# Optimization experiments

Hardware: AMD Instinct MI355X
Metric: run time of the kernel (lower is better)

## Reference

```python
import jax, jax.numpy as jnp
import numpy as np

KH = KW = 5  # receptive field


def _pair_w(a, b):
    # a, b: [...] in [0,1] -> soft one-hot over the 2-bit address (a = high bit): [..., 4]
    sa = jnp.stack([1.0 - a, a], axis=-1)
    sb = jnp.stack([1.0 - b, b], axis=-1)
    return (sa[..., :, None] * sb[..., None, :]).reshape(*a.shape, 4)


def _lut_nodes(g, lut):
    # g: [N, T, M, 6] node inputs in [0,1]; lut: [T, M, 64] raw LUT params.
    # DWN-style differentiable LUT: out = sum_a sigmoid(lut[a]) * prod_j (x_j if bit_j else 1-x_j)
    T, M = lut.shape[0], lut.shape[1]
    p = jax.nn.sigmoid(lut).reshape(T, M, 4, 4, 4)  # bits grouped pairwise, MSB-first
    Wa = _pair_w(g[..., 0], g[..., 1])  # [N,T,M,4]
    Wb = _pair_w(g[..., 2], g[..., 3])
    Wc = _pair_w(g[..., 4], g[..., 5])
    return jnp.einsum('tmpqr,ntmp,ntmq,ntmr->ntm', p, Wa, Wb, Wc)


def _lut_layer(h, idx, lut):
    # h: [N, T, P] previous-layer activations per tree; idx: [T, M, 6] in [0,P)
    T = idx.shape[0]
    g = h[:, jnp.arange(T)[:, None, None], idx]  # gather: [N, T, M, 6]
    return _lut_nodes(g, lut)


def setup_inputs() -> dict:
    key = jax.random.key(0)
    ks = jax.random.split(key, 7)
    x = jax.random.uniform(ks[0], (64, 1, 8, 8), dtype=jnp.float32)
    idx0 = jax.random.randint(ks[1], (128, 36, 6), 0, 25, dtype=jnp.int32)
    lut0 = jax.random.normal(ks[2], (128, 36, 64), dtype=jnp.float32)
    idx1 = jax.random.randint(ks[3], (128, 6, 6), 0, 36, dtype=jnp.int32)
    lut1 = jax.random.normal(ks[4], (128, 6, 64), dtype=jnp.float32)
    idx2 = jax.random.randint(ks[5], (128, 1, 6), 0, 6, dtype=jnp.int32)
    lut2 = jax.random.normal(ks[6], (128, 1, 64), dtype=jnp.float32)
    return dict(x=x, idx0=idx0, lut0=lut0, idx1=idx1, lut1=lut1, idx2=idx2, lut2=lut2)


def reference(x, idx0, lut0, idx1, lut1, idx2, lut2):
    B, C, H, W = x.shape
    oh, ow = H - KH + 1, W - KW + 1  # stride 1, padding 0 (as in nn.Unfold here)
    # im2col unfold, channel-major then (kh, kw) -- matches nn.Unfold ordering
    patches = jnp.stack(
        [x[:, c, i:i + oh, j:j + ow] for c in range(C) for i in range(KH) for j in range(KW)],
        axis=1,
    )  # [B, C*KH*KW, oh, ow]
    feat = patches.reshape(B, C * KH * KW, oh * ow).transpose(0, 2, 1).reshape(-1, C * KH * KW)  # [N, 25]
    # layer 0: gather from shared patch features into every tree
    g0 = feat[:, idx0]                      # [N, T, 36, 6]
    h0 = _lut_nodes(g0, lut0)               # [N, T, 36]
    h1 = _lut_layer(h0, idx1, lut1)         # [N, T, 6]
    h2 = _lut_layer(h1, idx2, lut2)         # [N, T, 1]
    T = lut0.shape[0]
    out = h2[..., 0].reshape(B, oh * ow, T).transpose(0, 2, 1).reshape(B, T, oh, ow)
    return out
```

## Files before the change

### kernel.cpp

```cpp
#include <hip/hip_runtime.h>
#include <hip/hip_fp16.h>

#define T_TREES 128
#define M0 36
#define M1 6
#define NNODES 43
#define XPAD 67
#define SLUT_ELEMS (T_TREES * NNODES * 64)

typedef float v2f __attribute__((ext_vector_type(2)));

__device__ __forceinline__ float sigmoidf(float v) {
    return 1.f / (1.f + __expf(-v));
}

__global__ __launch_bounds__(256) void sig_kernel(
    const float* __restrict__ lut0, const float* __restrict__ lut1,
    const float* __restrict__ lut2, float* __restrict__ slut) {
    int i4 = blockIdx.x * 256 + threadIdx.x;
    int j4 = i4 & 15;
    int tn = i4 >> 4;
    int t = tn / NNODES;
    int node = tn - t * NNODES;
    const float4* src;
    if (node < M0)            src = (const float4*)lut0 + (t * M0 + node) * 16 + j4;
    else if (node < M0 + M1)  src = (const float4*)lut1 + (t * M1 + (node - M0)) * 16 + j4;
    else                      src = (const float4*)lut2 + t * 16 + j4;
    float4 v = *src;
    float4 r;
    r.x = sigmoidf(v.x); r.y = sigmoidf(v.y);
    r.z = sigmoidf(v.z); r.w = sigmoidf(v.w);
    reinterpret_cast<float4*>(slut)[i4] = r;
}

__device__ __forceinline__ void pair_w(v2f a, v2f b, v2f w[4]) {
    v2f ab = a * b;
    w[3] = ab;
    w[2] = a - ab;
    w[1] = b - ab;
    w[0] = (1.f - a) - w[1];
}

__device__ __forceinline__ v2f lut_node_v2(const float* __restrict__ P,
                                           v2f a, v2f b, v2f c,
                                           v2f d, v2f e, v2f f) {
    v2f wa[4], wb[4], wc[4];
    pair_w(a, b, wa);
    pair_w(c, d, wb);
    pair_w(e, f, wc);
    v2f acc = {0.f, 0.f};
#pragma unroll
    for (int p = 0; p < 4; ++p) {
        v2f tp = {0.f, 0.f};
#pragma unroll
        for (int q = 0; q < 4; ++q) {
            const float* Pq = P + p * 16 + q * 4;
            v2f tq = Pq[0] * wc[0] + Pq[1] * wc[1] + Pq[2] * wc[2] + Pq[3] * wc[3];
            tp += tq * wb[q];
        }
        acc += tp * wa[p];
    }
    return acc;
}

__device__ __forceinline__ void hoist_P(const float* __restrict__ src, float P[64]) {
#pragma unroll
    for (int i = 0; i < 16; ++i) {
        float4 v = reinterpret_cast<const float4*>(src)[i];
        P[4 * i] = v.x; P[4 * i + 1] = v.y; P[4 * i + 2] = v.z; P[4 * i + 3] = v.w;
    }
}

__global__ __launch_bounds__(256, 4) void fused_kernel(
    const float* __restrict__ x,
    const int* __restrict__ idx0, const int* __restrict__ idx1,
    const int* __restrict__ idx2, const float* __restrict__ slut,
    float* __restrict__ out) {
    __shared__ float xs[8 * XPAD];
    __shared__ __half2 h0s[M0 * 64];
    __shared__ __align__(8) float h1s[M1 * 128];

    const int tid = threadIdx.x;
    const int bx = blockIdx.x;
    const int t = bx & 127;
    const int e = bx >> 7;

    const float* __restrict__ xq = x + e * 512;
    for (int i = tid; i < 512; i += 256)
        xs[(i >> 6) * XPAD + (i & 63)] = xq[i];
    __syncthreads();

    const int w = __builtin_amdgcn_readfirstlane(tid >> 6);
    const int ln = tid & 63;
    const float* __restrict__ slt = slut + t * (NNODES * 64);

#pragma unroll 1
    for (int k = 0; k < 9; ++k) {
        const int m = w * 9 + k;
        float P[64];
        hoist_P(slt + m * 64, P);
        const int* id = idx0 + (t * M0 + m) * 6;
        int di[6];
#pragma unroll
        for (int j = 0; j < 6; ++j) {
            int kk = id[j];
            int ii = (kk * 13) >> 6;
            di[j] = kk - 5 * ii + ii * 8;
        }
        int b = ln >> 3;
        int s = (ln & 7) * 2;
        int xb = b * XPAD + (s >> 2) * 8 + (s & 3);
        v2f g[6];
#pragma unroll
        for (int j = 0; j < 6; ++j) {
            int a0 = xb + di[j];
            g[j].x = xs[a0];
            g[j].y = xs[a0 + 1];
        }
        v2f r = lut_node_v2(P, g[0], g[1], g[2], g[3], g[4], g[5]);
        h0s[m * 64 + ln] = __floats2half2_rn(r.x, r.y);
    }
    __syncthreads();

#pragma unroll 1
    for (int m1 = w; m1 < M1; m1 += 4) {
        float P[64];
        hoist_P(slt + (M0 + m1) * 64, P);
        const int* id = idx1 + (t * M1 + m1) * 6;
        v2f g[6];
#pragma unroll
        for (int j = 0; j < 6; ++j) {
            float2 f = __half22float2(h0s[id[j] * 64 + ln]);
            g[j].x = f.x; g[j].y = f.y;
        }
        v2f r = lut_node_v2(P, g[0], g[1], g[2], g[3], g[4], g[5]);
        *reinterpret_cast<v2f*>(h1s + m1 * 128 + 2 * ln) = r;
    }
    __syncthreads();

    if (tid < 64) {
        float P[64];
        hoist_P(slt + (M0 + M1) * 64, P);
        const int* id = idx2 + t * 6;
        int rl = 2 * tid;
        v2f g[6];
#pragma unroll
        for (int j = 0; j < 6; ++j)
            g[j] = *reinterpret_cast<const v2f*>(h1s + id[j] * 128 + rl);
        v2f o = lut_node_v2(P, g[0], g[1], g[2], g[3], g[4], g[5]);
        int row = e * 128 + rl;
        int b = row >> 4, s = row & 15;
        *reinterpret_cast<v2f*>(out + b * (T_TREES * 16) + t * 16 + s) = o;
    }
}

__global__ __launch_bounds__(256, 2) void fused_fb_kernel(
    const float* __restrict__ x,
    const int* __restrict__ idx0, const float* __restrict__ lut0,
    const int* __restrict__ idx1, const float* __restrict__ lut1,
    const int* __restrict__ idx2, const float* __restrict__ lut2,
    float* __restrict__ out) {
    __shared__ float xs[16 * XPAD];
    __shared__ __align__(16) float Ps[NNODES * 64];
    __shared__ __half2 h0s[M0 * 128];
    __shared__ __align__(8) float h1s[M1 * 256];

    const int tid = threadIdx.x;
    const int bx = blockIdx.x;
    const int t = bx & 127;
    const int q = bx >> 7;

    const float* __restrict__ xq = x + q * 1024;
    for (int i = tid; i < 1024; i += 256)
        xs[(i >> 6) * XPAD + (i & 63)] = xq[i];
    for (int i = tid; i < NNODES * 64; i += 256) {
        float v;
        if (i < M0 * 64)              v = lut0[t * (M0 * 64) + i];
        else if (i < (M0 + M1) * 64)  v = lut1[t * (M1 * 64) + (i - M0 * 64)];
        else                          v = lut2[t * 64 + (i - (M0 + M1) * 64)];
        Ps[i] = sigmoidf(v);
    }
    __syncthreads();

    const int w = tid >> 6, ln = tid & 63;
#pragma unroll 1
    for (int k = 0; k < 9; ++k) {
        const int m = w * 9 + k;
        float P[64];
        hoist_P(Ps + m * 64, P);
        const int* id = idx0 + (t * M0 + m) * 6;
        int di[6];
#pragma unroll
        for (int j = 0; j < 6; ++j) {
            int kk = id[j];
            int ii = (kk * 13) >> 6;
            di[j] = kk - 5 * ii + ii * 8;
        }
#pragma unroll
        for (int u = 0; u < 2; ++u) {
            int p = u * 64 + ln;
            int b = p >> 3;
            int s = (p & 7) * 2;
            int xb = b * XPAD + (s >> 2) * 8 + (s & 3);
            v2f g[6];
#pragma unroll
            for (int j = 0; j < 6; ++j) {
                int a0 = xb + di[j];
                g[j].x = xs[a0];
                g[j].y = xs[a0 + 1];
            }
            v2f r = lut_node_v2(P, g[0], g[1], g[2], g[3], g[4], g[5]);
            h0s[m * 128 + p] = __floats2half2_rn(r.x, r.y);
        }
    }
    __syncthreads();
#pragma unroll 1
    for (int m1 = w; m1 < M1; m1 += 4) {
        float P[64];
        hoist_P(Ps + (M0 + m1) * 64, P);
        const int* id = idx1 + (t * M1 + m1) * 6;
#pragma unroll
        for (int u = 0; u < 2; ++u) {
            int p = u * 64 + ln;
            v2f g[6];
#pragma unroll
            for (int j = 0; j < 6; ++j) {
                float2 f = __half22float2(h0s[id[j] * 128 + p]);
                g[j].x = f.x; g[j].y = f.y;
            }
            v2f r = lut_node_v2(P, g[0], g[1], g[2], g[3], g[4], g[5]);
            *reinterpret_cast<v2f*>(h1s + m1 * 256 + 2 * p) = r;
        }
    }
    __syncthreads();
    if (tid < 128) {
        float P[64];
        hoist_P(Ps + (M0 + M1) * 64, P);
        const int* id = idx2 + t * 6;
        int rl = 2 * tid;
        v2f g[6];
#pragma unroll
        for (int j = 0; j < 6; ++j)
            g[j] = *reinterpret_cast<const v2f*>(h1s + id[j] * 256 + rl);
        v2f o = lut_node_v2(P, g[0], g[1], g[2], g[3], g[4], g[5]);
        int row = q * 256 + rl;
        int b = row >> 4, s = row & 15;
        *reinterpret_cast<v2f*>(out + b * (T_TREES * 16) + t * 16 + s) = o;
    }
}

extern "C" void kernel_launch(void* const* d_in, const int* in_sizes, int n_in,
                              void* d_out, int out_size, void* d_ws, size_t ws_size,
                              hipStream_t stream) {
    const float* x    = (const float*)d_in[0];
    const int*   idx0 = (const int*)  d_in[1];
    const float* lut0 = (const float*)d_in[2];
    const int*   idx1 = (const int*)  d_in[3];
    const float* lut1 = (const float*)d_in[4];
    const int*   idx2 = (const int*)  d_in[5];
    const float* lut2 = (const float*)d_in[6];
    float* out = (float*)d_out;

    if (ws_size >= (size_t)SLUT_ELEMS * sizeof(float)) {
        float* slut = (float*)d_ws;
        sig_kernel<<<SLUT_ELEMS / 4 / 256, 256, 0, stream>>>(lut0, lut1, lut2, slut);
        fused_kernel<<<dim3(8 * T_TREES), 256, 0, stream>>>(
            x, idx0, idx1, idx2, slut, out);
    } else {
        fused_fb_kernel<<<dim3(4 * T_TREES), 256, 0, stream>>>(
            x, idx0, lut0, idx1, lut1, idx2, lut2, out);
    }
}
```

Before: 24.25 us.

## Fuse sigmoid LUT precompute into main kernel with per-block workspace slice

Removes the separate sigmoid kernel launch. Each block now computes sigmoid of its tree's LUT parameters into its own slice of workspace memory, then reads them back through global memory. Blocks are halved and each handles twice the pixels, with two pixel groups per lane. This cuts one kernel launch and its dependency, but every block redundantly recomputes sigmoids (4x per tree). It also relies on a block fence so the block's own global writes are visible to its threads.

After: 23.79 us. About the same (-1.9%).

```diff
diff --git a/kernel.cpp b/kernel.cpp
--- a/kernel.cpp
+++ b/kernel.cpp
@@ -5,32 +5,13 @@
 #define M0 36
 #define M1 6
 #define NNODES 43
+#define TREE_SL (NNODES * 64)
 #define XPAD 67
-#define SLUT_ELEMS (T_TREES * NNODES * 64)
 
 typedef float v2f __attribute__((ext_vector_type(2)));
 
 __device__ __forceinline__ float sigmoidf(float v) {
     return 1.f / (1.f + __expf(-v));
-}
-
-__global__ __launch_bounds__(256) void sig_kernel(
-    const float* __restrict__ lut0, const float* __restrict__ lut1,
-    const float* __restrict__ lut2, float* __restrict__ slut) {
-    int i4 = blockIdx.x * 256 + threadIdx.x;
-    int j4 = i4 & 15;
-    int tn = i4 >> 4;
-    int t = tn / NNODES;
-    int node = tn - t * NNODES;
-    const float4* src;
-    if (node < M0)            src = (const float4*)lut0 + (t * M0 + node) * 16 + j4;
-    else if (node < M0 + M1)  src = (const float4*)lut1 + (t * M1 + (node - M0)) * 16 + j4;
-    else                      src = (const float4*)lut2 + t * 16 + j4;
-    float4 v = *src;
-    float4 r;
-    r.x = sigmoidf(v.x); r.y = sigmoidf(v.y);
-    r.z = sigmoidf(v.z); r.w = sigmoidf(v.w);
-    reinterpret_cast<float4*>(slut)[i4] = r;
 }
 
 __device__ __forceinline__ void pair_w(v2f a, v2f b, v2f w[4]) {
@@ -71,34 +52,44 @@
     }
 }
 
-__global__ __launch_bounds__(256, 4) void fused_kernel(
+__global__ __launch_bounds__(256) void fused_kernel(
     const float* __restrict__ x,
-    const int* __restrict__ idx0, const int* __restrict__ idx1,
-    const int* __restrict__ idx2, const float* __restrict__ slut,
-    float* __restrict__ out) {
-    __shared__ float xs[8 * XPAD];
-    __shared__ __half2 h0s[M0 * 64];
-    __shared__ __align__(8) float h1s[M1 * 128];
+    const int* __restrict__ idx0, const float* __restrict__ lut0,
+    const int* __restrict__ idx1, const float* __restrict__ lut1,
+    const int* __restrict__ idx2, const float* __restrict__ lut2,
+    float* __restrict__ ws_slut, float* __restrict__ out) {
+    __shared__ float xs[16 * XPAD];
+    __shared__ __half2 h0s[M0 * 128];
+    __shared__ __align__(8) float h1s[M1 * 256];
 
     const int tid = threadIdx.x;
     const int bx = blockIdx.x;
     const int t = bx & 127;
-    const int e = bx >> 7;
-
-    const float* __restrict__ xq = x + e * 512;
-    for (int i = tid; i < 512; i += 256)
+    const int q = bx >> 7;
+
+    float* __restrict__ slb = ws_slut + (size_t)bx * TREE_SL;
+
+    const float* __restrict__ xq = x + q * 1024;
+    for (int i = tid; i < 1024; i += 256)
         xs[(i >> 6) * XPAD + (i & 63)] = xq[i];
+    for (int i = tid; i < TREE_SL; i += 256) {
+        float v;
+        if (i < M0 * 64)              v = lut0[t * (M0 * 64) + i];
+        else if (i < (M0 + M1) * 64)  v = lut1[t * (M1 * 64) + (i - M0 * 64)];
+        else                          v = lut2[t * 64 + (i - (M0 + M1) * 64)];
+        slb[i] = sigmoidf(v);
+    }
+    __threadfence_block();
     __syncthreads();
 
     const int w = __builtin_amdgcn_readfirstlane(tid >> 6);
     const int ln = tid & 63;
-    const float* __restrict__ slt = slut + t * (NNODES * 64);
 
 #pragma unroll 1
     for (int k = 0; k < 9; ++k) {
         const int m = w * 9 + k;
         float P[64];
-        hoist_P(slt + m * 64, P);
+        hoist_P(slb + m * 64, P);
         const int* id = idx0 + (t * M0 + m) * 6;
         int di[6];
 #pragma unroll
@@ -107,48 +98,56 @@
             int ii = (kk * 13) >> 6;
             di[j] = kk - 5 * ii + ii * 8;
         }
-        int b = ln >> 3;
-        int s = (ln & 7) * 2;
-        int xb = b * XPAD + (s >> 2) * 8 + (s & 3);
-        v2f g[6];
-#pragma unroll
-        for (int j = 0; j < 6; ++j) {
-            int a0 = xb + di[j];
-            g[j].x = xs[a0];
-            g[j].y = xs[a0 + 1];
-        }
-        v2f r = lut_node_v2(P, g[0], g[1], g[2], g[3], g[4], g[5]);
-        h0s[m * 64 + ln] = __floats2half2_rn(r.x, r.y);
+#pragma unroll
+        for (int u = 0; u < 2; ++u) {
+            int p = u * 64 + ln;
+            int b = p >> 3;
+            int s = (p & 7) * 2;
+            int xb = b * XPAD + (s >> 2) * 8 + (s & 3);
+            v2f g[6];
+#pragma unroll
+            for (int j = 0; j < 6; ++j) {
+                int a0 = xb + di[j];
+                g[j].x = xs[a0];
+                g[j].y = xs[a0 + 1];
+            }
+            v2f r = lut_node_v2(P, g[0], g[1], g[2], g[3], g[4], g[5]);
+            h0s[m * 128 + p] = __floats2half2_rn(r.x, r.y);
+        }
     }
     __syncthreads();
 
 #pragma unroll 1
     for (int m1 = w; m1 < M1; m1 += 4) {
         float P[64];
-        hoist_P(slt + (M0 + m1) * 64, P);
+        hoist_P(slb + (M0 + m1) * 64, P);
         const int* id = idx1 + (t * M1 + m1) * 6;
-        v2f g[6];
-#pragma unroll
-        for (int j = 0; j < 6; ++j) {
-            float2 f = __half22float2(h0s[id[j] * 64 + ln]);
-            g[j].x = f.x; g[j].y = f.y;
-        }
-        v2f r = lut_node_v2(P, g[0], g[1], g[2], g[3], g[4], g[5]);
-        *reinterpret_cast<v2f*>(h1s + m1 * 128 + 2 * ln) = r;
-    }
-    __syncthreads();
-
-    if (tid < 64) {
-        float P[64];
-        hoist_P(slt + (M0 + M1) * 64, P);
+#pragma unroll
+        for (int u = 0; u < 2; ++u) {
+            int p = u * 64 + ln;
+            v2f g[6];
+#pragma unroll
+            for (int j = 0; j < 6; ++j) {
+                float2 f = __half22float2(h0s[id[j] * 128 + p]);
+                g[j].x = f.x; g[j].y = f.y;
+            }
+            v2f r = lut_node_v2(P, g[0], g[1], g[2], g[3], g[4], g[5]);
+            *reinterpret_cast<v2f*>(h1s + m1 * 256 + 2 * p) = r;
+        }
+    }
+    __syncthreads();
+
+    if (tid < 128) {
+        float P[64];
+        hoist_P(slb + (M0 + M1) * 64, P);
         const int* id = idx2 + t * 6;
         int rl = 2 * tid;
         v2f g[6];
 #pragma unroll
         for (int j = 0; j < 6; ++j)
-            g[j] = *reinterpret_cast<const v2f*>(h1s + id[j] * 128 + rl);
+            g[j] = *reinterpret_cast<const v2f*>(h1s + id[j] * 256 + rl);
         v2f o = lut_node_v2(P, g[0], g[1], g[2], g[3], g[4], g[5]);
-        int row = e * 128 + rl;
+        int row = q * 256 + rl;
         int b = row >> 4, s = row & 15;
         *reinterpret_cast<v2f*>(out + b * (T_TREES * 16) + t * 16 + s) = o;
     }
@@ -261,11 +260,10 @@
     const float* lut2 = (const float*)d_in[6];
     float* out = (float*)d_out;
 
-    if (ws_size >= (size_t)SLUT_ELEMS * sizeof(float)) {
-        float* slut = (float*)d_ws;
-        sig_kernel<<<SLUT_ELEMS / 4 / 256, 256, 0, stream>>>(lut0, lut1, lut2, slut);
-        fused_kernel<<<dim3(8 * T_TREES), 256, 0, stream>>>(
-            x, idx0, idx1, idx2, slut, out);
+    const size_t need = (size_t)512 * TREE_SL * sizeof(float);
+    if (ws_size >= need) {
+        fused_kernel<<<dim3(4 * T_TREES), 256, 0, stream>>>(
+            x, idx0, lut0, idx1, lut1, idx2, lut2, (float*)d_ws, out);
     } else {
         fused_fb_kernel<<<dim3(4 * T_TREES), 256, 0, stream>>>(
             x, idx0, lut0, idx1, lut1, idx2, lut2, out);
```
